# Performance work log

Measured on AMD Instinct MI355X. Metric: run time of the kernel, lower is better.

The kernel has to match this reference:

```python
import jax, jax.numpy as jnp
import numpy as np

HIDDEN = 1536
N_EXPERTS = 8
TOP_K = 2
N_GROUP = 1
TOPK_GROUP = 1
SCALE = 1.0


def setup_inputs() -> dict:
    key = jax.random.key(0)
    k1, k2 = jax.random.split(key)
    hidden_states = jax.random.normal(k1, (4, 4096, HIDDEN), dtype=jnp.float32)
    weight = jax.random.normal(k2, (N_EXPERTS, HIDDEN), dtype=jnp.float32) * 0.02
    e_score_correction_bias = jnp.zeros((N_EXPERTS,), dtype=jnp.float32)
    return {"hidden_states": hidden_states, "weight": weight,
            "e_score_correction_bias": e_score_correction_bias}


def reference(hidden_states, weight, e_score_correction_bias):
    # flatten tokens: (B*S, H)
    hs = hidden_states.reshape(-1, HIDDEN).astype(jnp.float32)
    router_logits = hs @ weight.astype(jnp.float32).T          # (T, E)
    scores = jax.nn.sigmoid(router_logits)                      # (T, E)

    # --- grouped top-k index selection (no-grad path in original) ---
    scores_for_choice = scores + e_score_correction_bias[None, :]
    per_group = scores_for_choice.reshape(-1, N_GROUP, N_EXPERTS // N_GROUP)
    # group score = sum of top-2 expert scores within each group
    group_scores = jax.lax.top_k(per_group, 2)[0].sum(axis=-1)  # (T, n_group)
    group_idx = jax.lax.top_k(group_scores, TOPK_GROUP)[1]      # (T, topk_group)
    group_mask = jnp.sum(jax.nn.one_hot(group_idx, N_GROUP, dtype=scores.dtype), axis=1)  # (T, n_group)
    score_mask = jnp.broadcast_to(group_mask[:, :, None], per_group.shape).reshape(-1, N_EXPERTS)
    masked_scores = jnp.where(score_mask > 0, scores_for_choice, 0.0)
    topk_indices = jax.lax.top_k(masked_scores, TOP_K)[1]       # (T, top_k) int32

    # --- gather weights from raw scores and normalize ---
    topk_weights = jnp.take_along_axis(scores, topk_indices, axis=1)  # (T, top_k)
    topk_weights = topk_weights / (topk_weights.sum(axis=-1, keepdims=True) + 1e-20)
    topk_weights = topk_weights * SCALE
    return topk_indices, topk_weights
```

## Files before the change

### kernel.cpp

```cpp
#include <hip/hip_runtime.h>
#include <math.h>

#define HID 1536
#define NEXP 8
#define NF4 (HID / 4)
#define TOK_PER_BLOCK 32

__global__ __launch_bounds__(256) void router_topk_kernel(
    const float* __restrict__ hs,
    const float* __restrict__ wgt,
    const float* __restrict__ bias,
    float* __restrict__ out,
    int T)
{
    __shared__ float4 wlds[NEXP * NF4];

    const int tid = threadIdx.x;

    const float4* wg4 = reinterpret_cast<const float4*>(wgt);
    #pragma unroll
    for (int i = 0; i < (NEXP * NF4) / 256; ++i)
        wlds[tid + i * 256] = wg4[tid + i * 256];
    __syncthreads();

    const int lane  = tid & 63;
    const int wid   = tid >> 6;
    const int q     = lane & 7;
    const int tg    = lane >> 3;
    const int token = blockIdx.x * TOK_PER_BLOCK + wid * 8 + tg;

    const float4* hrow = reinterpret_cast<const float4*>(hs) + (size_t)token * NF4;

    float acc[NEXP];
    #pragma unroll
    for (int e = 0; e < NEXP; ++e) acc[e] = 0.0f;

    #pragma unroll
    for (int kk = 0; kk < 48; kk += 8) {
        float4 h[8];
        #pragma unroll
        for (int j = 0; j < 8; ++j)
            h[j] = hrow[(kk + j) * 8 + q];
        #pragma unroll
        for (int j = 0; j < 8; ++j) {
            #pragma unroll
            for (int e = 0; e < NEXP; ++e) {
                float4 wv = wlds[e * NF4 + (kk + j) * 8 + q];
                acc[e] = fmaf(h[j].x, wv.x, acc[e]);
                acc[e] = fmaf(h[j].y, wv.y, acc[e]);
                acc[e] = fmaf(h[j].z, wv.z, acc[e]);
                acc[e] = fmaf(h[j].w, wv.w, acc[e]);
            }
        }
    }

    #pragma unroll
    for (int m = 1; m <= 4; m <<= 1) {
        #pragma unroll
        for (int e = 0; e < NEXP; ++e)
            acc[e] += __shfl_xor(acc[e], m, 64);
    }

    float s[NEXP], sc[NEXP];
    #pragma unroll
    for (int e = 0; e < NEXP; ++e) {
        s[e]  = 1.0f / (1.0f + expf(-acc[e]));
        sc[e] = s[e] + bias[e];
    }

    int   i0 = 0;
    float v0 = sc[0], w0 = s[0];
    #pragma unroll
    for (int e = 1; e < NEXP; ++e)
        if (sc[e] > v0) { v0 = sc[e]; w0 = s[e]; i0 = e; }

    int   i1 = -1;
    float v1 = -3.4e38f, w1 = 0.0f;
    #pragma unroll
    for (int e = 0; e < NEXP; ++e)
        if (e != i0 && sc[e] > v1) { v1 = sc[e]; w1 = s[e]; i1 = e; }

    const float inv = 1.0f / (w0 + w1 + 1e-20f);

    if (token < T && q < 2) {
        const float idxv = (q == 0) ? (float)i0 : (float)i1;
        const float wv   = ((q == 0) ? w0 : w1) * inv;
        out[token * 2 + q]         = idxv;
        out[T * 2 + token * 2 + q] = wv;
    }
}

extern "C" void kernel_launch(void* const* d_in, const int* in_sizes, int n_in,
                              void* d_out, int out_size, void* d_ws, size_t ws_size,
                              hipStream_t stream)
{
    const float* hs   = (const float*)d_in[0];
    const float* wgt  = (const float*)d_in[1];
    const float* bias = (const float*)d_in[2];
    float* out = (float*)d_out;

    const int T = in_sizes[0] / HID;
    const int blocks = (T + TOK_PER_BLOCK - 1) / TOK_PER_BLOCK;
    router_topk_kernel<<<blocks, 256, 0, stream>>>(hs, wgt, bias, out, T);
}
```

Measured before the change: 149.4 us.

## Process two tokens per 16-lane group to reuse LDS weight loads

Lanes are regrouped from 8 lanes per token into 16 lanes handling two tokens each, so every weight float4 read from LDS feeds two tokens' accumulators. The aim is to halve LDS read traffic per FMA. The cost is double the accumulator registers and an extra shuffle-reduction stage. Each lane also now issues 12 global loads per chunk instead of 8, which may raise register pressure and lower occupancy.

After: 150.8 us. About the same (+0.9%).

```diff
diff --git a/kernel.cpp b/kernel.cpp
--- a/kernel.cpp
+++ b/kernel.cpp
@@ -4,7 +4,7 @@
 #define HID 1536
 #define NEXP 8
 #define NF4 (HID / 4)
-#define TOK_PER_BLOCK 32
+#define TOKS_PER_BLOCK 32
 
 __global__ __launch_bounds__(256) void router_topk_kernel(
     const float* __restrict__ hs,
@@ -23,70 +23,97 @@
         wlds[tid + i * 256] = wg4[tid + i * 256];
     __syncthreads();
 
-    const int lane  = tid & 63;
-    const int wid   = tid >> 6;
-    const int q     = lane & 7;
-    const int tg    = lane >> 3;
-    const int token = blockIdx.x * TOK_PER_BLOCK + wid * 8 + tg;
+    const int lane = tid & 63;
+    const int wid  = tid >> 6;
+    const int q    = lane & 15;
+    const int tg   = lane >> 4;
+    const int base = blockIdx.x * TOKS_PER_BLOCK + wid * 8;
+    const int tA   = base + tg;
+    const int tB   = base + tg + 4;
 
-    const float4* hrow = reinterpret_cast<const float4*>(hs) + (size_t)token * NF4;
+    const float4* rowA = reinterpret_cast<const float4*>(hs) + (size_t)tA * NF4;
+    const float4* rowB = reinterpret_cast<const float4*>(hs) + (size_t)tB * NF4;
 
-    float acc[NEXP];
+    float accA[NEXP], accB[NEXP];
     #pragma unroll
-    for (int e = 0; e < NEXP; ++e) acc[e] = 0.0f;
+    for (int e = 0; e < NEXP; ++e) { accA[e] = 0.0f; accB[e] = 0.0f; }
 
     #pragma unroll
-    for (int kk = 0; kk < 48; kk += 8) {
-        float4 h[8];
+    for (int c = 0; c < 4; ++c) {
+        float4 hA[6], hB[6];
         #pragma unroll
-        for (int j = 0; j < 8; ++j)
-            h[j] = hrow[(kk + j) * 8 + q];
+        for (int j = 0; j < 6; ++j) {
+            hA[j] = rowA[(c * 6 + j) * 16 + q];
+            hB[j] = rowB[(c * 6 + j) * 16 + q];
+        }
         #pragma unroll
-        for (int j = 0; j < 8; ++j) {
+        for (int j = 0; j < 6; ++j) {
             #pragma unroll
             for (int e = 0; e < NEXP; ++e) {
-                float4 wv = wlds[e * NF4 + (kk + j) * 8 + q];
-                acc[e] = fmaf(h[j].x, wv.x, acc[e]);
-                acc[e] = fmaf(h[j].y, wv.y, acc[e]);
-                acc[e] = fmaf(h[j].z, wv.z, acc[e]);
-                acc[e] = fmaf(h[j].w, wv.w, acc[e]);
+                const float4 wv = wlds[e * NF4 + (c * 6 + j) * 16 + q];
+                accA[e] = fmaf(hA[j].x, wv.x, accA[e]);
+                accA[e] = fmaf(hA[j].y, wv.y, accA[e]);
+                accA[e] = fmaf(hA[j].z, wv.z, accA[e]);
+                accA[e] = fmaf(hA[j].w, wv.w, accA[e]);
+                accB[e] = fmaf(hB[j].x, wv.x, accB[e]);
+                accB[e] = fmaf(hB[j].y, wv.y, accB[e]);
+                accB[e] = fmaf(hB[j].z, wv.z, accB[e]);
+                accB[e] = fmaf(hB[j].w, wv.w, accB[e]);
             }
         }
     }
 
     #pragma unroll
-    for (int m = 1; m <= 4; m <<= 1) {
+    for (int m = 1; m <= 8; m <<= 1) {
         #pragma unroll
-        for (int e = 0; e < NEXP; ++e)
-            acc[e] += __shfl_xor(acc[e], m, 64);
+        for (int e = 0; e < NEXP; ++e) {
+            accA[e] += __shfl_xor(accA[e], m, 64);
+            accB[e] += __shfl_xor(accB[e], m, 64);
+        }
     }
 
-    float s[NEXP], sc[NEXP];
+    float sA[NEXP], scA[NEXP], sB[NEXP], scB[NEXP];
     #pragma unroll
     for (int e = 0; e < NEXP; ++e) {
-        s[e]  = 1.0f / (1.0f + expf(-acc[e]));
-        sc[e] = s[e] + bias[e];
+        const float be = bias[e];
+        sA[e]  = 1.0f / (1.0f + expf(-accA[e]));
+        scA[e] = sA[e] + be;
+        sB[e]  = 1.0f / (1.0f + expf(-accB[e]));
+        scB[e] = sB[e] + be;
     }
 
-    int   i0 = 0;
-    float v0 = sc[0], w0 = s[0];
+    int   a0 = 0;
+    float av0 = scA[0], aw0 = sA[0];
     #pragma unroll
     for (int e = 1; e < NEXP; ++e)
-        if (sc[e] > v0) { v0 = sc[e]; w0 = s[e]; i0 = e; }
-
-    int   i1 = -1;
-    float v1 = -3.4e38f, w1 = 0.0f;
+        if (scA[e] > av0) { av0 = scA[e]; aw0 = sA[e]; a0 = e; }
+    int   a1 = -1;
+    float av1 = -3.4e38f, aw1 = 0.0f;
     #pragma unroll
     for (int e = 0; e < NEXP; ++e)
-        if (e != i0 && sc[e] > v1) { v1 = sc[e]; w1 = s[e]; i1 = e; }
+        if (e != a0 && scA[e] > av1) { av1 = scA[e]; aw1 = sA[e]; a1 = e; }
+    const float ainv = 1.0f / (aw0 + aw1 + 1e-20f);
 
-    const float inv = 1.0f / (w0 + w1 + 1e-20f);
+    int   b0 = 0;
+    float bv0 = scB[0], bw0 = sB[0];
+    #pragma unroll
+    for (int e = 1; e < NEXP; ++e)
+        if (scB[e] > bv0) { bv0 = scB[e]; bw0 = sB[e]; b0 = e; }
+    int   b1 = -1;
+    float bv1 = -3.4e38f, bw1 = 0.0f;
+    #pragma unroll
+    for (int e = 0; e < NEXP; ++e)
+        if (e != b0 && scB[e] > bv1) { bv1 = scB[e]; bw1 = sB[e]; b1 = e; }
+    const float binv = 1.0f / (bw0 + bw1 + 1e-20f);
 
-    if (token < T && q < 2) {
-        const float idxv = (q == 0) ? (float)i0 : (float)i1;
-        const float wv   = ((q == 0) ? w0 : w1) * inv;
-        out[token * 2 + q]         = idxv;
-        out[T * 2 + token * 2 + q] = wv;
+    if (q < 2 && tA < T) {
+        out[tA * 2 + q]         = (q == 0) ? (float)a0 : (float)a1;
+        out[T * 2 + tA * 2 + q] = ((q == 0) ? aw0 : aw1) * ainv;
+    }
+    if (q >= 2 && q < 4 && tB < T) {
+        const int p = q - 2;
+        out[tB * 2 + p]         = (p == 0) ? (float)b0 : (float)b1;
+        out[T * 2 + tB * 2 + p] = ((p == 0) ? bw0 : bw1) * binv;
     }
 }
 
@@ -100,6 +127,6 @@
     float* out = (float*)d_out;
 
     const int T = in_sizes[0] / HID;
-    const int blocks = (T + TOK_PER_BLOCK - 1) / TOK_PER_BLOCK;
+    const int blocks = (T + TOKS_PER_BLOCK - 1) / TOKS_PER_BLOCK;
     router_topk_kernel<<<blocks, 256, 0, stream>>>(hs, wgt, bias, out, T);
 }
```
